# Performance work log

Hardware: AMD Instinct MI355X
Metric: run time of the kernel (lower is better)

The kernel has to match this reference:

```python
import jax, jax.numpy as jnp
import numpy as np

ALPHA = 0.1   # GCN2Conv initial-residual strength
THETA = 0.5   # GCN2Conv identity-mapping strength
NUM_LAYERS = 3
N_GRAPHS = 256


def setup_inputs() -> dict:
    key = jax.random.key(0)
    ks = jax.random.split(key, 8)
    N, E, IN, HID, OUT = 50000, 800000, 128, 64, 10
    x = jax.random.normal(ks[0], (N, IN), dtype=jnp.float32)
    edge_index = jax.random.randint(ks[1], (2, E), 0, N, dtype=jnp.int64)
    batch = jnp.sort(jax.random.randint(ks[2], (N,), 0, N_GRAPHS, dtype=jnp.int64))
    s_in = 1.0 / np.sqrt(IN)
    s_h = 1.0 / np.sqrt(HID)
    lin1_w = jax.random.uniform(ks[3], (IN, HID), jnp.float32, -s_in, s_in)
    lin1_b = jax.random.uniform(ks[4], (HID,), jnp.float32, -s_in, s_in)
    conv_ws = jax.random.uniform(ks[5], (NUM_LAYERS, HID, HID), jnp.float32, -s_h, s_h)
    lin2_w = jax.random.uniform(ks[6], (HID, OUT), jnp.float32, -s_h, s_h)
    lin2_b = jax.random.uniform(ks[7], (OUT,), jnp.float32, -s_h, s_h)
    return {"x": x, "edge_index": edge_index, "batch": batch,
            "lin1_w": lin1_w, "lin1_b": lin1_b, "conv_ws": conv_ws,
            "lin2_w": lin2_w, "lin2_b": lin2_b}


def reference(x, edge_index, batch, lin1_w, lin1_b, conv_ws, lin2_w, lin2_b):
    n = x.shape[0]
    # gcn_norm: add self-loops, symmetric deg^-1/2 normalization
    loops = jnp.arange(n, dtype=edge_index.dtype)
    row = jnp.concatenate([edge_index[0], loops])  # source nodes
    col = jnp.concatenate([edge_index[1], loops])  # target nodes
    deg = jax.ops.segment_sum(jnp.ones_like(row, dtype=x.dtype), col, num_segments=n)
    dinv = jnp.where(deg > 0, jax.lax.rsqrt(jnp.maximum(deg, 1.0)), 0.0)
    norm = dinv[row] * dinv[col]  # [E+N]

    h = jax.nn.relu(x @ lin1_w + lin1_b)  # [N, HID]
    h0 = h
    for i in range(conv_ws.shape[0]):
        beta = float(np.log(THETA / (i + 1) + 1.0))
        # sparse neighbor aggregation: gather messages, segment-sum at targets
        msgs = h[row] * norm[:, None]                     # [E+N, HID]
        agg = jax.ops.segment_sum(msgs, col, num_segments=n)
        s = (1.0 - ALPHA) * agg + ALPHA * h0              # initial residual
        h = jax.nn.relu((1.0 - beta) * s + beta * (s @ conv_ws[i]))

    # global_mean_pool over batch ids
    sums = jax.ops.segment_sum(h, batch, num_segments=N_GRAPHS)
    counts = jax.ops.segment_sum(jnp.ones((n,), x.dtype), batch, num_segments=N_GRAPHS)
    pooled = sums / jnp.maximum(counts, 1.0)[:, None]     # [N_GRAPHS, HID]
    return pooled @ lin2_w + lin2_b
```

## Files before the change

### kernel.cpp

```cpp
#include <hip/hip_runtime.h>
#include <hip/hip_fp16.h>
#include <math.h>

constexpr int IN_F = 128;
constexpr int HID  = 64;
constexpr int OUT_F = 10;
constexpr int NG   = 256;
constexpr int BSH  = 7;
constexpr int BNODES = 1 << BSH;
constexpr int CAP  = 3072;
constexpr int NBUK_MAX = 1024;
constexpr int EPB  = 8192;
constexpr int EMAX = 1024;

typedef _Float16 half8 __attribute__((ext_vector_type(8)));
typedef float f32x4 __attribute__((ext_vector_type(4)));

__global__ void k_detect(const unsigned int* w, int nwords, int* flag) {
    __shared__ int nz;
    if (threadIdx.x == 0) nz = 0;
    __syncthreads();
    int seen = 0;
    for (int i = 1 + 2 * (int)threadIdx.x; i < nwords; i += 2 * (int)blockDim.x)
        if (w[i] != 0u) seen = 1;
    if (seen) atomicOr(&nz, 1);
    __syncthreads();
    if (threadIdx.x == 0) *flag = (nz == 0) ? 1 : 0;
}

__device__ __forceinline__ int ld_idx(const void* p, long long i, int is64) {
    return is64 ? (int)((const long long*)p)[i] : ((const int*)p)[i];
}

__global__ __launch_bounds__(1024) void k_bucket2(const void* eidx, const int* f64,
                                                  int E, int nbuk,
                                                  int* gcur, unsigned* bucketed) {
    __shared__ int lhist[NBUK_MAX];
    __shared__ int lofs[NBUK_MAX];
    __shared__ int lcur[NBUK_MAX];
    __shared__ unsigned stage[EPB];
    __shared__ unsigned short sbid[EPB];
    int tid = threadIdx.x;
    long long base = (long long)blockIdx.x * EPB;
    int nval = (int)min((long long)EPB, (long long)E - base);
    int is64 = *f64;
    lhist[tid] = 0; lcur[tid] = 0;
    __syncthreads();
    unsigned pv[8]; int bv[8];
    #pragma unroll
    for (int j = 0; j < 8; ++j) {
        long long e = base + j * 1024 + tid;
        if (e < E) {
            int r = ld_idx(eidx, e, is64);
            int c = ld_idx(eidx, (long long)E + e, is64);
            int b = c >> BSH;
            pv[j] = (unsigned)r | ((unsigned)(c & (BNODES - 1)) << 20);
            bv[j] = b;
            atomicAdd(&lhist[b], 1);
        } else bv[j] = -1;
    }
    __syncthreads();
    lofs[tid] = lhist[tid];
    __syncthreads();
    for (int off = 1; off < NBUK_MAX; off <<= 1) {
        int v = (tid >= off) ? lofs[tid - off] : 0;
        __syncthreads();
        lofs[tid] += v;
        __syncthreads();
    }
    int cnt = lhist[tid];
    if (tid < nbuk && cnt > 0)
        lhist[tid] = atomicAdd(&gcur[tid], cnt);
    #pragma unroll
    for (int j = 0; j < 8; ++j) {
        if (bv[j] >= 0) {
            int b = bv[j];
            int ex = (b > 0) ? lofs[b - 1] : 0;
            int p = ex + atomicAdd(&lcur[b], 1);
            stage[p] = pv[j];
            sbid[p] = (unsigned short)b;
        }
    }
    __syncthreads();
    for (int p = tid; p < nval; p += 1024) {
        int b = sbid[p];
        int ex = (b > 0) ? lofs[b - 1] : 0;
        int dst = lhist[b] + (p - ex);
        if (dst < CAP)
            bucketed[(long long)b * CAP + dst] = stage[p];
    }
}

__global__ void k_bucket_fb(const void* eidx, const int* f64, int E,
                            int* gcur, unsigned* bucketed) {
    int e = blockIdx.x * blockDim.x + threadIdx.x;
    if (e >= E) return;
    int is64 = *f64;
    int r = ld_idx(eidx, e, is64);
    int c = ld_idx(eidx, (long long)E + e, is64);
    int b = c >> BSH;
    int pos = atomicAdd(&gcur[b], 1);
    if (pos < CAP)
        bucketed[(long long)b * CAP + pos] =
            (unsigned)r | ((unsigned)(c & (BNODES - 1)) << 20);
}

__global__ __launch_bounds__(512) void k_bscan(const int* __restrict__ gcur,
                                               int* __restrict__ gofs, int nbuk,
                                               int* rowptr, int N) {
    __shared__ int tot[512];
    int tid = threadIdx.x;
    int chunk = (nbuk + 511) / 512;
    int st = tid * chunk, en = min(st + chunk, nbuk);
    int s = 0;
    for (int i = st; i < en; ++i) s += min(gcur[i], CAP);
    tot[tid] = s;
    __syncthreads();
    for (int off = 1; off < 512; off <<= 1) {
        int a = (tid >= off) ? tot[tid - off] : 0;
        __syncthreads();
        tot[tid] += a;
        __syncthreads();
    }
    int run = tot[tid] - s;
    for (int i = st; i < en; ++i) { gofs[i] = run; run += min(gcur[i], CAP); }
    if (tid == 511) rowptr[N] = tot[511];
}

__global__ __launch_bounds__(256) void k_bfill(const int* __restrict__ gcur,
                                               const int* __restrict__ gofs,
                                               const unsigned* __restrict__ bucketed,
                                               int* __restrict__ rowptr,
                                               float* __restrict__ dinv,
                                               int* __restrict__ csr_src, int N) {
    __shared__ int lhist[BNODES], lrp[BNODES], lcur[BNODES];
    __shared__ int stage[CAP];
    int b = blockIdx.x;
    int cnt = min(gcur[b], CAP);
    int base = gofs[b];
    int nb0 = b << BSH;
    int tid = threadIdx.x;
    const unsigned* bk = bucketed + (long long)b * CAP;
    if (tid < BNODES) { lhist[tid] = 0; lcur[tid] = 0; }
    __syncthreads();
    for (int t = tid; t < cnt; t += 256) atomicAdd(&lhist[bk[t] >> 20], 1);
    __syncthreads();
    if (tid < BNODES) lrp[tid] = lhist[tid];
    __syncthreads();
    for (int off = 1; off < BNODES; off <<= 1) {
        int a = (tid < BNODES && tid >= off) ? lrp[tid - off] : 0;
        __syncthreads();
        if (tid < BNODES) lrp[tid] += a;
        __syncthreads();
    }
    if (tid < BNODES) {
        int ex = lrp[tid] - lhist[tid];
        lrp[tid] = ex;
        int node = nb0 + tid;
        if (node < N) {
            rowptr[node] = base + ex;
            dinv[node] = rsqrtf((float)lhist[tid] + 1.0f);
        }
    }
    __syncthreads();
    for (int t = tid; t < cnt; t += 256) {
        unsigned v = bk[t];
        int lc = v >> 20;
        int q = atomicAdd(&lcur[lc], 1);
        stage[lrp[lc] + q] = (int)(v & 0xFFFFFu);
    }
    __syncthreads();
    for (int t = tid; t < cnt; t += 256) csr_src[base + t] = stage[t];
}

constexpr int NBK = 16;
__global__ __launch_bounds__(256) void k_lin1(const float* __restrict__ x,
                                              const float* __restrict__ w1,
                                              const float* __restrict__ b1,
                                              const float* __restrict__ dinv,
                                              unsigned short* __restrict__ h0,
                                              unsigned short* __restrict__ hs0, int N) {
    __shared__ float xs[NBK][IN_F];
    int nb0 = blockIdx.x * NBK;
    for (int t = threadIdx.x; t < NBK * (IN_F / 4); t += 256) {
        int n = t >> 5, k4 = t & 31;
        int gn = nb0 + n;
        float4 v = make_float4(0.f, 0.f, 0.f, 0.f);
        if (gn < N) v = ((const float4*)x)[(long long)gn * (IN_F / 4) + k4];
        *(float4*)&xs[n][k4 * 4] = v;
    }
    __syncthreads();
    int wv = threadIdx.x >> 6;
    int c  = threadIdx.x & 63;
    int n0 = wv * 4;
    float bias = b1[c];
    float a0 = bias, a1 = bias, a2 = bias, a3 = bias;
    #pragma unroll 4
    for (int k = 0; k < IN_F; k += 4) {
        float w_0 = w1[(k + 0) * HID + c];
        float w_1 = w1[(k + 1) * HID + c];
        float w_2 = w1[(k + 2) * HID + c];
        float w_3 = w1[(k + 3) * HID + c];
        float4 x0 = *(float4*)&xs[n0 + 0][k];
        float4 x1 = *(float4*)&xs[n0 + 1][k];
        float4 x2 = *(float4*)&xs[n0 + 2][k];
        float4 x3 = *(float4*)&xs[n0 + 3][k];
        a0 = fmaf(x0.x, w_0, a0); a0 = fmaf(x0.y, w_1, a0);
        a0 = fmaf(x0.z, w_2, a0); a0 = fmaf(x0.w, w_3, a0);
        a1 = fmaf(x1.x, w_0, a1); a1 = fmaf(x1.y, w_1, a1);
        a1 = fmaf(x1.z, w_2, a1); a1 = fmaf(x1.w, w_3, a1);
        a2 = fmaf(x2.x, w_0, a2); a2 = fmaf(x2.y, w_1, a2);
        a2 = fmaf(x2.z, w_2, a2); a2 = fmaf(x2.w, w_3, a2);
        a3 = fmaf(x3.x, w_0, a3); a3 = fmaf(x3.y, w_1, a3);
        a3 = fmaf(x3.z, w_2, a3); a3 = fmaf(x3.w, w_3, a3);
    }
    float acc[4] = {a0, a1, a2, a3};
    #pragma unroll
    for (int n = 0; n < 4; ++n) {
        int gn = nb0 + n0 + n;
        if (gn < N) {
            float r = fmaxf(acc[n], 0.f);
            __half hr = __float2half(r);
            __half hs = __float2half(r * dinv[gn]);
            h0 [(long long)gn * HID + c] = *(unsigned short*)&hr;
            hs0[(long long)gn * HID + c] = *(unsigned short*)&hs;
        }
    }
}

__global__ __launch_bounds__(256) void k_layer(const int* __restrict__ rowptr,
                                               const int* __restrict__ csr_src,
                                               const float* __restrict__ dinv,
                                               const unsigned short* __restrict__ hs_in,
                                               const unsigned short* __restrict__ h0,
                                               const float* __restrict__ W,
                                               float beta, int scale_out,
                                               unsigned short* __restrict__ h_out, int N) {
    __shared__ unsigned short s_lds[16][HID];
    __shared__ unsigned short wt_lds[HID][HID];
    __shared__ int ldsidx[EMAX];
    __shared__ int lrowp[17];
    int tid = threadIdx.x;
    int l = tid & 63, wv = tid >> 6;
    int nb = blockIdx.x * 16;

    if (tid < 17) lrowp[tid] = rowptr[min(nb + tid, N)];
    #pragma unroll
    for (int jw = 0; jw < 4; ++jw) {
        int f = (jw * 256 + tid) * 4;
        int k = f >> 6, n0 = f & 63;
        float4 wv4 = *(const float4*)&W[f];
        int slot = (k >> 3);
        int kk = k & 7;
        wt_lds[n0 + 0][((slot ^ ((n0 + 0) & 7)) * 8) + kk] = (unsigned short)__half_as_ushort(__float2half(wv4.x));
        wt_lds[n0 + 1][((slot ^ ((n0 + 1) & 7)) * 8) + kk] = (unsigned short)__half_as_ushort(__float2half(wv4.y));
        wt_lds[n0 + 2][((slot ^ ((n0 + 2) & 7)) * 8) + kk] = (unsigned short)__half_as_ushort(__float2half(wv4.z));
        wt_lds[n0 + 3][((slot ^ ((n0 + 3) & 7)) * 8) + kk] = (unsigned short)__half_as_ushort(__float2half(wv4.w));
    }
    __syncthreads();

    int eblk0 = lrowp[0];
    int ecnt = lrowp[16] - eblk0;
    bool use_lds = (ecnt <= EMAX);
    if (use_lds)
        for (int t = tid; t < ecnt; t += 256) ldsidx[t] = csr_src[eblk0 + t];
    __syncthreads();

    const uint4* hin4 = (const uint4*)hs_in;
    const uint4* h04  = (const uint4*)h0;
    int j = l >> 4, q = (l >> 3) & 1, m = l & 7;
    int row = wv * 4 + j;
    int node = nb + row;
    int e0 = lrowp[row], e1 = lrowp[row + 1];

    __half2 a[4] = {__half2(0.f, 0.f), __half2(0.f, 0.f),
                    __half2(0.f, 0.f), __half2(0.f, 0.f)};
    if (use_lds) {
        for (int e = e0 + q; e < e1; e += 2) {
            int r = ldsidx[e - eblk0];
            uint4 v = hin4[(long long)r * 8 + m];
            const __half2* p = (const __half2*)&v;
            #pragma unroll
            for (int jj = 0; jj < 4; ++jj) a[jj] = __hadd2(a[jj], p[jj]);
        }
    } else {
        for (int e = e0 + q; e < e1; e += 2) {
            int r = csr_src[e];
            uint4 v = hin4[(long long)r * 8 + m];
            const __half2* p = (const __half2*)&v;
            #pragma unroll
            for (int jj = 0; jj < 4; ++jj) a[jj] = __hadd2(a[jj], p[jj]);
        }
    }
    #pragma unroll
    for (int jj = 0; jj < 4; ++jj) {
        unsigned t = __shfl_xor(*(unsigned*)&a[jj], 8, 64);
        a[jj] = __hadd2(a[jj], *(__half2*)&t);
    }
    if (q == 0) {
        if (node < N) {
            float di = dinv[node];
            uint4 hv = hin4[(long long)node * 8 + m];
            uint4 rv = h04 [(long long)node * 8 + m];
            const __half2* hp = (const __half2*)&hv;
            const __half2* rp = (const __half2*)&rv;
            __attribute__((aligned(16))) unsigned short out8[8];
            #pragma unroll
            for (int jj = 0; jj < 4; ++jj) {
                __half2 t = __hadd2(a[jj], hp[jj]);
                float slo = fmaf(0.9f * di, __low2float(t),  0.1f * __low2float(rp[jj]));
                float shi = fmaf(0.9f * di, __high2float(t), 0.1f * __high2float(rp[jj]));
                *(__half2*)&out8[jj * 2] = __floats2half2_rn(slo, shi);
            }
            int slot = m ^ (row & 7);
            *(uint4*)&s_lds[row][slot * 8] = *(uint4*)out8;
        } else {
            int slot = m ^ (row & 7);
            uint4 z = make_uint4(0, 0, 0, 0);
            *(uint4*)&s_lds[row][slot * 8] = z;
        }
    }
    __syncthreads();

    int i16 = l & 15, kc = l >> 4;
    f32x4 acc = {0.f, 0.f, 0.f, 0.f};
    #pragma unroll
    for (int ks = 0; ks < 2; ++ks) {
        int cb = ks * 4 + kc;
        int sa = cb ^ (i16 & 7);
        half8 av = *(half8*)&s_lds[i16][sa * 8];
        int n = wv * 16 + i16;
        int sb = cb ^ (n & 7);
        half8 bv = *(half8*)&wt_lds[n][sb * 8];
        acc = __builtin_amdgcn_mfma_f32_16x16x32_f16(av, bv, acc, 0, 0, 0);
    }
    #pragma unroll
    for (int r = 0; r < 4; ++r) {
        int orow = kc * 4 + r;
        int onode = nb + orow;
        if (onode < N) {
            int colg = wv * 16 + i16;
            int slot = (colg >> 3) ^ (orow & 7);
            __half sh = *(__half*)&s_lds[orow][slot * 8 + (colg & 7)];
            float sv = __half2float(sh);
            float v = fmaxf(sv + beta * (acc[r] - sv), 0.f);
            if (scale_out) v *= dinv[onode];
            __half hv2 = __float2half(v);
            h_out[(long long)onode * HID + colg] = *(unsigned short*)&hv2;
        }
    }
}

constexpr int POOL_CHUNK = 256;
__global__ __launch_bounds__(256) void k_pool(const unsigned short* __restrict__ h,
                                              const void* batch, const int* f64,
                                              float* psum, float* pcnt, int N) {
    int c = threadIdx.x & 63;
    int g = threadIdx.x >> 6;
    int n0 = blockIdx.x * POOL_CHUNK;
    int nend = min(n0 + POOL_CHUNK, N);
    int is64 = *f64;
    float sum = 0.f;
    int cnt = 0, curb = -1;
    for (int n = n0 + g; n < nend; n += 4) {
        int b = ld_idx(batch, n, is64);
        if (b != curb) {
            if (curb >= 0) {
                atomicAdd(&psum[(long long)curb * HID + c], sum);
                if (c == 0) atomicAdd(&pcnt[curb], (float)cnt);
            }
            curb = b; sum = 0.f; cnt = 0;
        }
        __half hv = *(__half*)&h[(long long)n * HID + c];
        sum += __half2float(hv);
        cnt++;
    }
    if (curb >= 0) {
        atomicAdd(&psum[(long long)curb * HID + c], sum);
        if (c == 0) atomicAdd(&pcnt[curb], (float)cnt);
    }
}

__global__ void k_out(const float* __restrict__ psum, const float* __restrict__ pcnt,
                      const float* __restrict__ w2, const float* __restrict__ b2,
                      float* __restrict__ out) {
    int g = blockIdx.x;
    int tid = threadIdx.x;
    __shared__ float pr[HID];
    float cnt = fmaxf(pcnt[g], 1.0f);
    pr[tid] = psum[(long long)g * HID + tid] / cnt;
    __syncthreads();
    if (tid < OUT_F) {
        float acc = b2[tid];
        #pragma unroll
        for (int k = 0; k < HID; ++k)
            acc = fmaf(pr[k], w2[k * OUT_F + tid], acc);
        out[g * OUT_F + tid] = acc;
    }
}

static inline size_t align256(size_t x) { return (x + 255) & ~(size_t)255; }

extern "C" void kernel_launch(void* const* d_in, const int* in_sizes, int n_in,
                              void* d_out, int out_size, void* d_ws, size_t ws_size,
                              hipStream_t stream) {
    const float* x     = (const float*)d_in[0];
    const void*  eidx  = d_in[1];
    const void*  batch = d_in[2];
    const float* w1    = (const float*)d_in[3];
    const float* b1    = (const float*)d_in[4];
    const float* convw = (const float*)d_in[5];
    const float* w2    = (const float*)d_in[6];
    const float* b2    = (const float*)d_in[7];
    float* out = (float*)d_out;

    int N = in_sizes[0] / IN_F;
    int E = in_sizes[1] / 2;
    int nbuk = (N + BNODES - 1) >> BSH;

    char* ws = (char*)d_ws;
    float* dinv    = (float*)ws;                ws += align256((size_t)N * 4);
    unsigned short* h0  = (unsigned short*)ws;  ws += align256((size_t)N * HID * 2);
    unsigned short* hs0 = (unsigned short*)ws;  ws += align256((size_t)N * HID * 2);
    unsigned short* hb  = (unsigned short*)ws;  ws += align256((size_t)N * HID * 2);
    float* psum    = (float*)ws;                ws += align256((size_t)NG * HID * 4);
    float* pcnt    = (float*)ws;                ws += align256((size_t)NG * 4);
    int*   rowptr  = (int*)ws;                  ws += align256((size_t)(N + 1) * 4);
    int*   csr_src = (int*)ws;                  ws += align256((size_t)E * 4);
    int*   gcur    = (int*)ws;                  ws += align256((size_t)nbuk * 4);
    int*   gofs    = (int*)ws;                  ws += align256((size_t)(nbuk + 1) * 4);
    unsigned* bucketed = (unsigned*)ws;         ws += align256((size_t)nbuk * CAP * 4);
    int*   flag    = (int*)ws;

    k_detect<<<1, 256, 0, stream>>>((const unsigned int*)eidx, 4096, flag);

    hipMemsetAsync(gcur, 0, (size_t)nbuk * 4, stream);
    if (nbuk <= NBUK_MAX)
        k_bucket2<<<(E + EPB - 1) / EPB, 1024, 0, stream>>>(eidx, flag, E, nbuk,
                                                            gcur, bucketed);
    else
        k_bucket_fb<<<(E + 255) / 256, 256, 0, stream>>>(eidx, flag, E, gcur, bucketed);
    k_bscan<<<1, 512, 0, stream>>>(gcur, gofs, nbuk, rowptr, N);
    k_bfill<<<nbuk, 256, 0, stream>>>(gcur, gofs, bucketed, rowptr, dinv, csr_src, N);

    k_lin1<<<(N + NBK - 1) / NBK, 256, 0, stream>>>(x, w1, b1, dinv, h0, hs0, N);

    int nlb = (N + 15) / 16;
    float beta0 = logf(0.5f / 1.0f + 1.0f);
    float beta1 = logf(0.5f / 2.0f + 1.0f);
    float beta2 = logf(0.5f / 3.0f + 1.0f);
    k_layer<<<nlb, 256, 0, stream>>>(rowptr, csr_src, dinv, hs0, h0,
                                     convw + 0 * HID * HID, beta0, 1, hb, N);
    k_layer<<<nlb, 256, 0, stream>>>(rowptr, csr_src, dinv, hb, h0,
                                     convw + 1 * HID * HID, beta1, 1, hs0, N);
    k_layer<<<nlb, 256, 0, stream>>>(rowptr, csr_src, dinv, hs0, h0,
                                     convw + 2 * HID * HID, beta2, 0, hb, N);

    hipMemsetAsync(psum, 0, ((size_t)NG * HID + NG) * 4, stream);
    k_pool<<<(N + POOL_CHUNK - 1) / POOL_CHUNK, 256, 0, stream>>>(hb, batch, flag,
                                                                  psum, pcnt, N);
    k_out<<<NG, 64, 0, stream>>>(psum, pcnt, w2, b2, out);
}
```

Before: 159.3 us.

## Use MFMA fp16 for lin1 and unroll gather loop by two edges

Rewrites the input linear layer to convert x and W1 to fp16 in swizzled LDS tiles and compute with 16x16x32 MFMA instructions over 64-node blocks, replacing scalar FMA loops. Separately, the layer kernel's neighbor-gather loop now issues two independent row loads per iteration to increase memory-level parallelism. The first reduces compute and per-block overhead in lin1 at the cost of fp16 rounding of x and the weights. The second may raise register pressure.

```diff
diff --git a/kernel.cpp b/kernel.cpp
--- a/kernel.cpp
+++ b/kernel.cpp
@@ -173,57 +173,79 @@
     for (int t = tid; t < cnt; t += 256) csr_src[base + t] = stage[t];
 }
 
-constexpr int NBK = 16;
+constexpr int LNB = 64;
 __global__ __launch_bounds__(256) void k_lin1(const float* __restrict__ x,
                                               const float* __restrict__ w1,
                                               const float* __restrict__ b1,
                                               const float* __restrict__ dinv,
                                               unsigned short* __restrict__ h0,
                                               unsigned short* __restrict__ hs0, int N) {
-    __shared__ float xs[NBK][IN_F];
-    int nb0 = blockIdx.x * NBK;
-    for (int t = threadIdx.x; t < NBK * (IN_F / 4); t += 256) {
-        int n = t >> 5, k4 = t & 31;
-        int gn = nb0 + n;
-        float4 v = make_float4(0.f, 0.f, 0.f, 0.f);
-        if (gn < N) v = ((const float4*)x)[(long long)gn * (IN_F / 4) + k4];
-        *(float4*)&xs[n][k4 * 4] = v;
-    }
-    __syncthreads();
-    int wv = threadIdx.x >> 6;
-    int c  = threadIdx.x & 63;
-    int n0 = wv * 4;
-    float bias = b1[c];
-    float a0 = bias, a1 = bias, a2 = bias, a3 = bias;
-    #pragma unroll 4
-    for (int k = 0; k < IN_F; k += 4) {
-        float w_0 = w1[(k + 0) * HID + c];
-        float w_1 = w1[(k + 1) * HID + c];
-        float w_2 = w1[(k + 2) * HID + c];
-        float w_3 = w1[(k + 3) * HID + c];
-        float4 x0 = *(float4*)&xs[n0 + 0][k];
-        float4 x1 = *(float4*)&xs[n0 + 1][k];
-        float4 x2 = *(float4*)&xs[n0 + 2][k];
-        float4 x3 = *(float4*)&xs[n0 + 3][k];
-        a0 = fmaf(x0.x, w_0, a0); a0 = fmaf(x0.y, w_1, a0);
-        a0 = fmaf(x0.z, w_2, a0); a0 = fmaf(x0.w, w_3, a0);
-        a1 = fmaf(x1.x, w_0, a1); a1 = fmaf(x1.y, w_1, a1);
-        a1 = fmaf(x1.z, w_2, a1); a1 = fmaf(x1.w, w_3, a1);
-        a2 = fmaf(x2.x, w_0, a2); a2 = fmaf(x2.y, w_1, a2);
-        a2 = fmaf(x2.z, w_2, a2); a2 = fmaf(x2.w, w_3, a2);
-        a3 = fmaf(x3.x, w_0, a3); a3 = fmaf(x3.y, w_1, a3);
-        a3 = fmaf(x3.z, w_2, a3); a3 = fmaf(x3.w, w_3, a3);
-    }
-    float acc[4] = {a0, a1, a2, a3};
-    #pragma unroll
-    for (int n = 0; n < 4; ++n) {
-        int gn = nb0 + n0 + n;
+    __shared__ unsigned short xs[LNB][IN_F];
+    __shared__ unsigned short wt[HID][IN_F];
+    int tid = threadIdx.x;
+    int l = tid & 63, wv = tid >> 6;
+    int nb0 = blockIdx.x * LNB;
+
+    for (int t = tid; t < (IN_F * HID / 4); t += 256) {
+        int k = t >> 4;
+        int n0 = (t & 15) * 4;
+        float4 v = *(const float4*)&w1[k * HID + n0];
+        int kc = k >> 3, ke = k & 7;
+        wt[n0 + 0][((kc ^ ((n0 + 0) & 15)) * 8) + ke] = __half_as_ushort(__float2half(v.x));
+        wt[n0 + 1][((kc ^ ((n0 + 1) & 15)) * 8) + ke] = __half_as_ushort(__float2half(v.y));
+        wt[n0 + 2][((kc ^ ((n0 + 2) & 15)) * 8) + ke] = __half_as_ushort(__float2half(v.z));
+        wt[n0 + 3][((kc ^ ((n0 + 3) & 15)) * 8) + ke] = __half_as_ushort(__float2half(v.w));
+    }
+    for (int t = tid; t < LNB * (IN_F / 8); t += 256) {
+        int row = t >> 4, kc = t & 15;
+        int gn = nb0 + row;
+        float4 va = make_float4(0.f, 0.f, 0.f, 0.f), vb = va;
         if (gn < N) {
-            float r = fmaxf(acc[n], 0.f);
-            __half hr = __float2half(r);
-            __half hs = __float2half(r * dinv[gn]);
-            h0 [(long long)gn * HID + c] = *(unsigned short*)&hr;
-            hs0[(long long)gn * HID + c] = *(unsigned short*)&hs;
+            va = ((const float4*)x)[(long long)gn * 32 + kc * 2];
+            vb = ((const float4*)x)[(long long)gn * 32 + kc * 2 + 1];
+        }
+        __attribute__((aligned(16))) unsigned short t8[8];
+        t8[0] = __half_as_ushort(__float2half(va.x));
+        t8[1] = __half_as_ushort(__float2half(va.y));
+        t8[2] = __half_as_ushort(__float2half(va.z));
+        t8[3] = __half_as_ushort(__float2half(va.w));
+        t8[4] = __half_as_ushort(__float2half(vb.x));
+        t8[5] = __half_as_ushort(__float2half(vb.y));
+        t8[6] = __half_as_ushort(__float2half(vb.z));
+        t8[7] = __half_as_ushort(__float2half(vb.w));
+        int slot = kc ^ (row & 15);
+        *(uint4*)&xs[row][slot * 8] = *(uint4*)t8;
+    }
+    __syncthreads();
+
+    int i16 = l & 15, hk = l >> 4;
+    f32x4 acc0 = {0.f,0.f,0.f,0.f}, acc1 = acc0, acc2 = acc0, acc3 = acc0;
+    #pragma unroll
+    for (int kc4 = 0; kc4 < 4; ++kc4) {
+        int kc = kc4 * 4 + hk;
+        int arow = wv * 16 + i16;
+        half8 av = *(half8*)&xs[arow][(kc ^ (arow & 15)) * 8];
+        half8 b0 = *(half8*)&wt[ 0 + i16][(kc ^ (( 0 + i16) & 15)) * 8];
+        half8 b1v = *(half8*)&wt[16 + i16][(kc ^ ((16 + i16) & 15)) * 8];
+        half8 b2v = *(half8*)&wt[32 + i16][(kc ^ ((32 + i16) & 15)) * 8];
+        half8 b3v = *(half8*)&wt[48 + i16][(kc ^ ((48 + i16) & 15)) * 8];
+        acc0 = __builtin_amdgcn_mfma_f32_16x16x32_f16(av, b0,  acc0, 0, 0, 0);
+        acc1 = __builtin_amdgcn_mfma_f32_16x16x32_f16(av, b1v, acc1, 0, 0, 0);
+        acc2 = __builtin_amdgcn_mfma_f32_16x16x32_f16(av, b2v, acc2, 0, 0, 0);
+        acc3 = __builtin_amdgcn_mfma_f32_16x16x32_f16(av, b3v, acc3, 0, 0, 0);
+    }
+    #pragma unroll
+    for (int r = 0; r < 4; ++r) {
+        int gn = nb0 + wv * 16 + hk * 4 + r;
+        if (gn >= N) continue;
+        float di = dinv[gn];
+        float vr[4] = {acc0[r], acc1[r], acc2[r], acc3[r]};
+        #pragma unroll
+        for (int ct = 0; ct < 4; ++ct) {
+            int col = ct * 16 + i16;
+            float v = fmaxf(vr[ct] + b1[col], 0.f);
+            h0 [(long long)gn * HID + col] = __half_as_ushort(__float2half(v));
+            hs0[(long long)gn * HID + col] = __half_as_ushort(__float2half(v * di));
         }
     }
 }
@@ -252,10 +274,10 @@
         float4 wv4 = *(const float4*)&W[f];
         int slot = (k >> 3);
         int kk = k & 7;
-        wt_lds[n0 + 0][((slot ^ ((n0 + 0) & 7)) * 8) + kk] = (unsigned short)__half_as_ushort(__float2half(wv4.x));
-        wt_lds[n0 + 1][((slot ^ ((n0 + 1) & 7)) * 8) + kk] = (unsigned short)__half_as_ushort(__float2half(wv4.y));
-        wt_lds[n0 + 2][((slot ^ ((n0 + 2) & 7)) * 8) + kk] = (unsigned short)__half_as_ushort(__float2half(wv4.z));
-        wt_lds[n0 + 3][((slot ^ ((n0 + 3) & 7)) * 8) + kk] = (unsigned short)__half_as_ushort(__float2half(wv4.w));
+        wt_lds[n0 + 0][((slot ^ ((n0 + 0) & 7)) * 8) + kk] = __half_as_ushort(__float2half(wv4.x));
+        wt_lds[n0 + 1][((slot ^ ((n0 + 1) & 7)) * 8) + kk] = __half_as_ushort(__float2half(wv4.y));
+        wt_lds[n0 + 2][((slot ^ ((n0 + 2) & 7)) * 8) + kk] = __half_as_ushort(__float2half(wv4.z));
+        wt_lds[n0 + 3][((slot ^ ((n0 + 3) & 7)) * 8) + kk] = __half_as_ushort(__float2half(wv4.w));
     }
     __syncthreads();
 
@@ -275,18 +297,41 @@
 
     __half2 a[4] = {__half2(0.f, 0.f), __half2(0.f, 0.f),
                     __half2(0.f, 0.f), __half2(0.f, 0.f)};
+    int e = e0 + q;
     if (use_lds) {
-        for (int e = e0 + q; e < e1; e += 2) {
-            int r = ldsidx[e - eblk0];
-            uint4 v = hin4[(long long)r * 8 + m];
+        for (; e + 2 < e1; e += 4) {
+            int r0 = ldsidx[e - eblk0];
+            int r1 = ldsidx[e + 2 - eblk0];
+            uint4 v0 = hin4[(long long)r0 * 8 + m];
+            uint4 v1 = hin4[(long long)r1 * 8 + m];
+            const __half2* p0 = (const __half2*)&v0;
+            const __half2* p1 = (const __half2*)&v1;
+            #pragma unroll
+            for (int jj = 0; jj < 4; ++jj) a[jj] = __hadd2(a[jj], p0[jj]);
+            #pragma unroll
+            for (int jj = 0; jj < 4; ++jj) a[jj] = __hadd2(a[jj], p1[jj]);
+        }
+        if (e < e1) {
+            uint4 v = hin4[(long long)ldsidx[e - eblk0] * 8 + m];
             const __half2* p = (const __half2*)&v;
             #pragma unroll
             for (int jj = 0; jj < 4; ++jj) a[jj] = __hadd2(a[jj], p[jj]);
         }
     } else {
-        for (int e = e0 + q; e < e1; e += 2) {
-            int r = csr_src[e];
-            uint4 v = hin4[(long long)r * 8 + m];
+        for (; e + 2 < e1; e += 4) {
+            int r0 = csr_src[e];
+            int r1 = csr_src[e + 2];
+            uint4 v0 = hin4[(long long)r0 * 8 + m];
+            uint4 v1 = hin4[(long long)r1 * 8 + m];
+            const __half2* p0 = (const __half2*)&v0;
+            const __half2* p1 = (const __half2*)&v1;
+            #pragma unroll
+            for (int jj = 0; jj < 4; ++jj) a[jj] = __hadd2(a[jj], p0[jj]);
+            #pragma unroll
+            for (int jj = 0; jj < 4; ++jj) a[jj] = __hadd2(a[jj], p1[jj]);
+        }
+        if (e < e1) {
+            uint4 v = hin4[(long long)csr_src[e] * 8 + m];
             const __half2* p = (const __half2*)&v;
             #pragma unroll
             for (int jj = 0; jj < 4; ++jj) a[jj] = __hadd2(a[jj], p[jj]);
@@ -443,7 +488,7 @@
     k_bscan<<<1, 512, 0, stream>>>(gcur, gofs, nbuk, rowptr, N);
     k_bfill<<<nbuk, 256, 0, stream>>>(gcur, gofs, bucketed, rowptr, dinv, csr_src, N);
 
-    k_lin1<<<(N + NBK - 1) / NBK, 256, 0, stream>>>(x, w1, b1, dinv, h0, hs0, N);
+    k_lin1<<<(N + LNB - 1) / LNB, 256, 0, stream>>>(x, w1, b1, dinv, h0, hs0, N);
 
     int nlb = (N + 15) / 16;
     float beta0 = logf(0.5f / 1.0f + 1.0f);
```

Result: faster. 141.6 us (-11.1%).
